# Optimization experiments

Hardware: AMD Instinct MI355X
Metric: run time of the kernel (lower is better)

Reference implementation:

```python
import jax, jax.numpy as jnp
import numpy as np

N = 50000      # nodes
E = 800000     # edges (avg degree 16)
DIN = 128
DH = 128
DOUT = 40
ALPHA = 0.1
BETA = 1.0


def gcn_conv(x, src, dst, ew, W, b, n):
    """PyG GCNConv: add self-loops, symmetric deg^-1/2 normalization, gather-scatter."""
    idx = jnp.arange(n)
    s = jnp.concatenate([src, idx])
    d = jnp.concatenate([dst, idx])
    w = jnp.concatenate([ew, jnp.ones((n,), x.dtype)])
    deg = jax.ops.segment_sum(w, d, num_segments=n)            # [N]
    dinv = jnp.where(deg > 0, jax.lax.rsqrt(deg), 0.0)
    norm = dinv[s] * w * dinv[d]                               # [E+N]
    h = x @ W                                                  # [N, dout]
    msg = h[s] * norm[:, None]                                 # gather + scale
    out = jax.ops.segment_sum(msg, d, num_segments=n)          # scatter-add
    return out + b


def setup_inputs() -> dict:
    key = jax.random.key(0)
    ks = jax.random.split(key, 10)
    x = jax.random.normal(ks[0], (N, DIN), jnp.float32)
    edge_index = jax.random.randint(ks[1], (2, E), 0, N, dtype=jnp.int64)
    edge_weight = jax.random.uniform(ks[2], (E,), jnp.float32)
    W1 = jax.random.normal(ks[3], (DIN, DH), jnp.float32) / np.float32(np.sqrt(DIN))
    b1 = jnp.zeros((DH,), jnp.float32)
    W2 = jax.random.normal(ks[4], (DH, DH), jnp.float32) / np.float32(np.sqrt(DH))
    b2 = jnp.zeros((DH,), jnp.float32)
    W3 = jax.random.normal(ks[5], (DH, DOUT), jnp.float32) / np.float32(np.sqrt(DH))
    b3 = jnp.zeros((DOUT,), jnp.float32)
    return {"x": x, "edge_index": edge_index, "edge_weight": edge_weight,
            "W1": W1, "b1": b1, "W2": W2, "b2": b2, "W3": W3, "b3": b3}


def reference(x, edge_index, edge_weight, W1, b1, W2, b2, W3, b3):
    src, dst = edge_index[0], edge_index[1]
    ones_w = jnp.ones((E,), x.dtype)
    h1 = jax.nn.relu(gcn_conv(x, src, dst, ones_w, W1, b1, N))   # conv1 (edge_weight=None)
    hc = gcn_conv(h1, src, dst, edge_weight, W2, b2, N)          # crf_layer with edge_weight
    h = ALPHA * h1 + BETA * hc                                   # weighted residual combo
    # LearnableBernoulliDropout: identity in eval mode
    out = gcn_conv(h, src, dst, ones_w, W3, b3, N)               # conv2
    return jax.nn.log_softmax(out, axis=1)
```

## Files before the change

kernel.cpp:

```cpp
#include <hip/hip_runtime.h>
#include <math.h>

#define DIN  128
#define DH   128
#define DOUT 40
#define ALPHA_C 0.1f
#define BETA_C  1.0f
#define SLOT 64

typedef __attribute__((ext_vector_type(8))) short short8;
typedef __attribute__((ext_vector_type(4))) float floatx4;

static inline int cdiv_h(int a, int b) { return (a + b - 1) / b; }

static __device__ __forceinline__ unsigned short f2b(float f) {
    unsigned u = __float_as_uint(f);
    u = u + 0x7FFFu + ((u >> 16) & 1u);
    return (unsigned short)(u >> 16);
}
static __device__ __forceinline__ unsigned pk2(float x, float y) {
    return (unsigned)f2b(x) | ((unsigned)f2b(y) << 16);
}
static __device__ __forceinline__ float2 b2f2(unsigned u) {
    float2 r;
    r.x = __uint_as_float(u << 16);
    r.y = __uint_as_float(u & 0xFFFF0000u);
    return r;
}

__global__ __launch_bounds__(256) void build_slots(const int* __restrict__ src,
                                                   const int* __restrict__ dst,
                                                   const float* __restrict__ ew,
                                                   int* cnt,
                                                   int* __restrict__ csr_src,
                                                   float* __restrict__ csr_w, int E) {
    int e = blockIdx.x * 256 + threadIdx.x;
    if (e >= E) return;
    int d = dst[e];
    int pos = atomicAdd(&cnt[d], 1);
    if (pos < SLOT) {
        int base = (d << 6) + pos;
        csr_src[base] = src[e];
        csr_w[base] = ew[e];
    }
}

__global__ __launch_bounds__(256) void wdeg_dinv(const int* __restrict__ cnt,
                                                 const float* __restrict__ csr_w,
                                                 float* __restrict__ dinv1,
                                                 float* __restrict__ dinv2, int n) {
    int i = blockIdx.x * 256 + threadIdx.x;
    if (i >= n) return;
    int c = cnt[i]; if (c > SLOT) c = SLOT;
    dinv1[i] = rsqrtf((float)c + 1.f);
    float s = 1.f;
    int jb = i << 6;
    for (int j = 0; j < c; ++j) s += csr_w[jb + j];
    dinv2[i] = rsqrtf(s);
}

template <bool ABF16>
__global__ __launch_bounds__(256) void gemm128(const void* __restrict__ Ain,
                                               const float* __restrict__ W,
                                               unsigned short* __restrict__ C, int M) {
    __shared__ short As[128 * 128];
    __shared__ short Bs[128 * 128];
    int t = threadIdx.x;
    int blockM = blockIdx.x * 128;

    {
        int r = t >> 1, h = t & 1;
        int rg = blockM + r; if (rg > M - 1) rg = M - 1;
        if (ABF16) {
            const uint4* arow = (const uint4*)((const unsigned short*)Ain + (size_t)rg * 128);
            #pragma unroll
            for (int i = 0; i < 8; ++i) {
                int chunk = h * 8 + i;
                uint4 v = arow[chunk];
                *(uint4*)&As[r * 128 + ((chunk ^ (r & 7)) * 8)] = v;
            }
        } else {
            const float4* arow = (const float4*)((const float*)Ain + (size_t)rg * 128);
            #pragma unroll
            for (int i = 0; i < 8; ++i) {
                int chunk = h * 8 + i;
                float4 v0 = arow[chunk * 2], v1 = arow[chunk * 2 + 1];
                uint4 p;
                p.x = pk2(v0.x, v0.y); p.y = pk2(v0.z, v0.w);
                p.z = pk2(v1.x, v1.y); p.w = pk2(v1.z, v1.w);
                *(uint4*)&As[r * 128 + ((chunk ^ (r & 7)) * 8)] = p;
            }
        }
    }
    {
        int n = t & 127;
        int k0 = (t >> 7) * 64;
        #pragma unroll
        for (int it = 0; it < 8; ++it) {
            int k = k0 + it * 8;
            float f0 = W[(size_t)(k + 0) * 128 + n];
            float f1 = W[(size_t)(k + 1) * 128 + n];
            float f2 = W[(size_t)(k + 2) * 128 + n];
            float f3 = W[(size_t)(k + 3) * 128 + n];
            float f4 = W[(size_t)(k + 4) * 128 + n];
            float f5 = W[(size_t)(k + 5) * 128 + n];
            float f6 = W[(size_t)(k + 6) * 128 + n];
            float f7 = W[(size_t)(k + 7) * 128 + n];
            uint4 p;
            p.x = pk2(f0, f1); p.y = pk2(f2, f3);
            p.z = pk2(f4, f5); p.w = pk2(f6, f7);
            *(uint4*)&Bs[n * 128 + (((k >> 3) ^ (n & 7)) * 8)] = p;
        }
    }
    __syncthreads();

    int w = t >> 6, l = t & 63;
    int q = l >> 4, lm = l & 15;
    int rowoff = (w >> 1) * 64, coloff = (w & 1) * 64;

    floatx4 acc[4][4] = {};
    #pragma unroll
    for (int ks = 0; ks < 4; ++ks) {
        int chunk = ks * 4 + q;
        int sw = (chunk ^ (lm & 7)) * 8;
        short8 af[4], bf[4];
        #pragma unroll
        for (int tm = 0; tm < 4; ++tm)
            af[tm] = *(const short8*)&As[(rowoff + tm * 16 + lm) * 128 + sw];
        #pragma unroll
        for (int tn = 0; tn < 4; ++tn)
            bf[tn] = *(const short8*)&Bs[(coloff + tn * 16 + lm) * 128 + sw];
        #pragma unroll
        for (int tm = 0; tm < 4; ++tm)
            #pragma unroll
            for (int tn = 0; tn < 4; ++tn)
                acc[tm][tn] = __builtin_amdgcn_mfma_f32_16x16x32_bf16(af[tm], bf[tn], acc[tm][tn], 0, 0, 0);
    }

    #pragma unroll
    for (int tm = 0; tm < 4; ++tm) {
        #pragma unroll
        for (int reg = 0; reg < 4; ++reg) {
            int row = blockM + rowoff + tm * 16 + q * 4 + reg;
            if (row >= M) continue;
            #pragma unroll
            for (int tn = 0; tn < 4; ++tn) {
                int col = coloff + tn * 16 + lm;
                C[(size_t)row * 128 + col] = f2b(acc[tm][tn][reg]);
            }
        }
    }
}

__global__ __launch_bounds__(256) void gemm40_lsm(const unsigned short* __restrict__ Ain,
                                                  const float* __restrict__ W,
                                                  const float* __restrict__ bias,
                                                  float* __restrict__ out, int M) {
    __shared__ short As[128 * 128];
    __shared__ short Bs[48 * 128];
    int t = threadIdx.x;
    int blockM = blockIdx.x * 128;

    {
        int r = t >> 1, h = t & 1;
        int rg = blockM + r; if (rg > M - 1) rg = M - 1;
        const uint4* arow = (const uint4*)(Ain + (size_t)rg * 128);
        #pragma unroll
        for (int i = 0; i < 8; ++i) {
            int chunk = h * 8 + i;
            uint4 v = arow[chunk];
            *(uint4*)&As[r * 128 + ((chunk ^ (r & 7)) * 8)] = v;
        }
    }
    {
        int n = t & 63;
        int k0 = (t >> 6) * 32;
        #pragma unroll
        for (int it = 0; it < 4; ++it) {
            int k = k0 + it * 8;
            uint4 p = {0, 0, 0, 0};
            if (n < 40) {
                float f0 = W[(size_t)(k + 0) * 40 + n];
                float f1 = W[(size_t)(k + 1) * 40 + n];
                float f2 = W[(size_t)(k + 2) * 40 + n];
                float f3 = W[(size_t)(k + 3) * 40 + n];
                float f4 = W[(size_t)(k + 4) * 40 + n];
                float f5 = W[(size_t)(k + 5) * 40 + n];
                float f6 = W[(size_t)(k + 6) * 40 + n];
                float f7 = W[(size_t)(k + 7) * 40 + n];
                p.x = pk2(f0, f1); p.y = pk2(f2, f3);
                p.z = pk2(f4, f5); p.w = pk2(f6, f7);
            }
            if (n < 48)
                *(uint4*)&Bs[n * 128 + (((k >> 3) ^ (n & 7)) * 8)] = p;
        }
    }
    __syncthreads();

    int w = t >> 6, l = t & 63;
    int q = l >> 4, lm = l & 15;
    int rowoff = w * 32;

    floatx4 acc[2][3] = {};
    #pragma unroll
    for (int ks = 0; ks < 4; ++ks) {
        int chunk = ks * 4 + q;
        int sw = (chunk ^ (lm & 7)) * 8;
        short8 af[2], bf[3];
        #pragma unroll
        for (int tm = 0; tm < 2; ++tm)
            af[tm] = *(const short8*)&As[(rowoff + tm * 16 + lm) * 128 + sw];
        #pragma unroll
        for (int tn = 0; tn < 3; ++tn)
            bf[tn] = *(const short8*)&Bs[(tn * 16 + lm) * 128 + sw];
        #pragma unroll
        for (int tm = 0; tm < 2; ++tm)
            #pragma unroll
            for (int tn = 0; tn < 3; ++tn)
                acc[tm][tn] = __builtin_amdgcn_mfma_f32_16x16x32_bf16(af[tm], bf[tn], acc[tm][tn], 0, 0, 0);
    }

    float bb0 = bias[lm];
    float bb1 = bias[16 + lm];
    float bb2 = (lm < 8) ? bias[32 + lm] : 0.f;
    #pragma unroll
    for (int tm = 0; tm < 2; ++tm) {
        #pragma unroll
        for (int reg = 0; reg < 4; ++reg) {
            int row = blockM + rowoff + tm * 16 + q * 4 + reg;
            float v0 = acc[tm][0][reg] + bb0;
            float v1 = acc[tm][1][reg] + bb1;
            float v2 = (lm < 8) ? acc[tm][2][reg] + bb2 : -INFINITY;
            float mx = fmaxf(fmaxf(v0, v1), v2);
            #pragma unroll
            for (int o = 1; o < 16; o <<= 1) mx = fmaxf(mx, __shfl_xor(mx, o, 64));
            float ss = expf(v0 - mx) + expf(v1 - mx) + ((lm < 8) ? expf(v2 - mx) : 0.f);
            #pragma unroll
            for (int o = 1; o < 16; o <<= 1) ss += __shfl_xor(ss, o, 64);
            float ls = mx + logf(ss);
            if (row < M) {
                out[(size_t)row * 40 + lm]      = v0 - ls;
                out[(size_t)row * 40 + 16 + lm] = v1 - ls;
                if (lm < 8) out[(size_t)row * 40 + 32 + lm] = v2 - ls;
            }
        }
    }
}

template <int MODE>
__global__ __launch_bounds__(256) void agg128(const unsigned short* __restrict__ hpre,
                                              unsigned short* __restrict__ io,
                                              const float* __restrict__ bias,
                                              const float* __restrict__ dinv,
                                              const int* __restrict__ cnt,
                                              const int* __restrict__ csr_src,
                                              const float* __restrict__ csr_w, int n) {
    int row = blockIdx.x * 4 + (threadIdx.x >> 6);
    if (row >= n) return;
    int lane = threadIdx.x & 63;
    const unsigned* hp = (const unsigned*)hpre;

    float di = dinv[row];
    float d2 = di * di;
    float2 acc = b2f2(hp[(size_t)row * 64 + lane]);
    if (MODE == 2) {
        acc.x *= d2; acc.y *= d2;
    } else {
        float2 bb = ((const float2*)bias)[lane];
        acc.x = fmaf(acc.x, d2, bb.x);
        acc.y = fmaf(acc.y, d2, bb.y);
    }

    int c = cnt[row]; if (c > SLOT) c = SLOT;
    int jb = row << 6;
    int je = jb + c;
    int j = jb;

    while (j + 8 <= je) {
        int ss[8]; float2 ff[8];
        #pragma unroll
        for (int u = 0; u < 8; ++u) ss[u] = csr_src[j + u];
        #pragma unroll
        for (int u = 0; u < 8; ++u) ff[u] = b2f2(hp[(size_t)ss[u] * 64 + lane]);
        #pragma unroll
        for (int u = 0; u < 8; ++u) {
            float cc = (MODE == 1) ? dinv[ss[u]] * csr_w[j + u] * di : dinv[ss[u]] * di;
            acc.x = fmaf(cc, ff[u].x, acc.x);
            acc.y = fmaf(cc, ff[u].y, acc.y);
        }
        j += 8;
    }
    if (j + 4 <= je) {
        int ss[4]; float2 ff[4];
        #pragma unroll
        for (int u = 0; u < 4; ++u) ss[u] = csr_src[j + u];
        #pragma unroll
        for (int u = 0; u < 4; ++u) ff[u] = b2f2(hp[(size_t)ss[u] * 64 + lane]);
        #pragma unroll
        for (int u = 0; u < 4; ++u) {
            float cc = (MODE == 1) ? dinv[ss[u]] * csr_w[j + u] * di : dinv[ss[u]] * di;
            acc.x = fmaf(cc, ff[u].x, acc.x);
            acc.y = fmaf(cc, ff[u].y, acc.y);
        }
        j += 4;
    }
    for (; j < je; ++j) {
        int s0 = csr_src[j];
        float cc = (MODE == 1) ? dinv[s0] * csr_w[j] * di : dinv[s0] * di;
        float2 f0 = b2f2(hp[(size_t)s0 * 64 + lane]);
        acc.x = fmaf(cc, f0.x, acc.x);
        acc.y = fmaf(cc, f0.y, acc.y);
    }

    unsigned* iop = (unsigned*)io;
    if (MODE == 0) {
        acc.x = fmaxf(acc.x, 0.f); acc.y = fmaxf(acc.y, 0.f);
        iop[(size_t)row * 64 + lane] = pk2(acc.x, acc.y);
    } else if (MODE == 1) {
        float2 h1 = b2f2(iop[(size_t)row * 64 + lane]);
        acc.x = fmaf(ALPHA_C, h1.x, BETA_C * acc.x);
        acc.y = fmaf(ALPHA_C, h1.y, BETA_C * acc.y);
        iop[(size_t)row * 64 + lane] = pk2(acc.x, acc.y);
    } else {
        iop[(size_t)row * 64 + lane] = pk2(acc.x, acc.y);
    }
}

extern "C" void kernel_launch(void* const* d_in, const int* in_sizes, int n_in,
                              void* d_out, int out_size, void* d_ws, size_t ws_size,
                              hipStream_t stream) {
    const float* x   = (const float*)d_in[0];
    const int*   ei  = (const int*)  d_in[1];
    const float* ew  = (const float*)d_in[2];
    const float* W1  = (const float*)d_in[3];
    const float* b1  = (const float*)d_in[4];
    const float* W2  = (const float*)d_in[5];
    const float* b2  = (const float*)d_in[6];
    const float* W3  = (const float*)d_in[7];
    const float* b3  = (const float*)d_in[8];
    float* out = (float*)d_out;

    const int Nn = in_sizes[0] / DIN;
    const int E  = in_sizes[1] / 2;
    const int* src = ei;
    const int* dst = ei + E;

    char* wsb = (char*)d_ws;
    int*   cnt     = (int*)wsb;                          wsb += (size_t)Nn * 4;
    float* dinv1   = (float*)wsb;                        wsb += (size_t)Nn * 4;
    float* dinv2   = (float*)wsb;                        wsb += (size_t)Nn * 4;
    int*   csr_src = (int*)wsb;                          wsb += (size_t)Nn * SLOT * 4;
    float* csr_w   = (float*)wsb;                        wsb += (size_t)Nn * SLOT * 4;
    unsigned short* hpreb = (unsigned short*)wsb;        wsb += (size_t)Nn * DH * 2;
    unsigned short* h1b   = (unsigned short*)wsb;        wsb += (size_t)Nn * DH * 2;

    hipMemsetAsync(cnt, 0, (size_t)Nn * 4, stream);
    build_slots<<<cdiv_h(E, 256), 256, 0, stream>>>(src, dst, ew, cnt, csr_src, csr_w, E);
    wdeg_dinv<<<cdiv_h(Nn, 256), 256, 0, stream>>>(cnt, csr_w, dinv1, dinv2, Nn);

    int gemmGrid = cdiv_h(Nn, 128);
    int aggGrid = cdiv_h(Nn, 4);

    gemm128<false><<<gemmGrid, 256, 0, stream>>>(x, W1, hpreb, Nn);
    agg128<0><<<aggGrid, 256, 0, stream>>>(hpreb, h1b, b1, dinv1, cnt, csr_src, csr_w, Nn);

    gemm128<true><<<gemmGrid, 256, 0, stream>>>(h1b, W2, hpreb, Nn);
    agg128<1><<<aggGrid, 256, 0, stream>>>(hpreb, h1b, b2, dinv2, cnt, csr_src, csr_w, Nn);

    agg128<2><<<aggGrid, 256, 0, stream>>>(h1b, hpreb, b3, dinv1, cnt, csr_src, csr_w, Nn);
    gemm40_lsm<<<gemmGrid, 256, 0, stream>>>(hpreb, W3, b3, out, Nn);
}
```

Before: 290.1 us.

## Interleave CSR src/weight and split wave into four edge groups with 16B loads

The separate csr_src and csr_w arrays are merged into one interleaved int2 array, so a single load fetches both the source index and the weight. The aggregation kernel now splits each 64-lane wave into four groups of 16 lanes. Each group handles every fourth edge and loads a full 256-byte feature row with 16-byte vector loads, and the partial sums are combined with cross-lane shuffles. build_slots also handles two edges per thread. The aim is fewer, wider memory transactions and more edge-level parallelism per row, at the cost of more registers and the shuffle reduction.

```diff
diff --git a/kernel.cpp b/kernel.cpp
--- a/kernel.cpp
+++ b/kernel.cpp
@@ -32,21 +32,25 @@
                                                    const int* __restrict__ dst,
                                                    const float* __restrict__ ew,
                                                    int* cnt,
-                                                   int* __restrict__ csr_src,
-                                                   float* __restrict__ csr_w, int E) {
+                                                   int2* __restrict__ csr, int E) {
+    int half = (E + 1) >> 1;
     int e = blockIdx.x * 256 + threadIdx.x;
-    if (e >= E) return;
-    int d = dst[e];
-    int pos = atomicAdd(&cnt[d], 1);
-    if (pos < SLOT) {
-        int base = (d << 6) + pos;
-        csr_src[base] = src[e];
-        csr_w[base] = ew[e];
+    if (e >= half) return;
+    {
+        int d = dst[e];
+        int pos = atomicAdd(&cnt[d], 1);
+        if (pos < SLOT) { int2 r; r.x = src[e]; r.y = __float_as_int(ew[e]); csr[(d << 6) + pos] = r; }
+    }
+    int e2 = e + half;
+    if (e2 < E) {
+        int d = dst[e2];
+        int pos = atomicAdd(&cnt[d], 1);
+        if (pos < SLOT) { int2 r; r.x = src[e2]; r.y = __float_as_int(ew[e2]); csr[(d << 6) + pos] = r; }
     }
 }
 
 __global__ __launch_bounds__(256) void wdeg_dinv(const int* __restrict__ cnt,
-                                                 const float* __restrict__ csr_w,
+                                                 const int2* __restrict__ csr,
                                                  float* __restrict__ dinv1,
                                                  float* __restrict__ dinv2, int n) {
     int i = blockIdx.x * 256 + threadIdx.x;
@@ -55,7 +59,7 @@
     dinv1[i] = rsqrtf((float)c + 1.f);
     float s = 1.f;
     int jb = i << 6;
-    for (int j = 0; j < c; ++j) s += csr_w[jb + j];
+    for (int j = 0; j < c; ++j) s += __int_as_float(csr[jb + j].y);
     dinv2[i] = rsqrtf(s);
 }
 
@@ -253,76 +257,82 @@
                                               const float* __restrict__ bias,
                                               const float* __restrict__ dinv,
                                               const int* __restrict__ cnt,
-                                              const int* __restrict__ csr_src,
-                                              const float* __restrict__ csr_w, int n) {
+                                              const int2* __restrict__ csr, int n) {
     int row = blockIdx.x * 4 + (threadIdx.x >> 6);
     if (row >= n) return;
     int lane = threadIdx.x & 63;
-    const unsigned* hp = (const unsigned*)hpre;
+    int q = lane >> 4, m = lane & 15;
+    const uint4* hp4 = (const uint4*)hpre;
 
     float di = dinv[row];
-    float d2 = di * di;
-    float2 acc = b2f2(hp[(size_t)row * 64 + lane]);
-    if (MODE == 2) {
-        acc.x *= d2; acc.y *= d2;
-    } else {
-        float2 bb = ((const float2*)bias)[lane];
-        acc.x = fmaf(acc.x, d2, bb.x);
-        acc.y = fmaf(acc.y, d2, bb.y);
-    }
+    float acc[8] = {};
 
     int c = cnt[row]; if (c > SLOT) c = SLOT;
     int jb = row << 6;
     int je = jb + c;
-    int j = jb;
-
-    while (j + 8 <= je) {
-        int ss[8]; float2 ff[8];
-        #pragma unroll
-        for (int u = 0; u < 8; ++u) ss[u] = csr_src[j + u];
-        #pragma unroll
-        for (int u = 0; u < 8; ++u) ff[u] = b2f2(hp[(size_t)ss[u] * 64 + lane]);
-        #pragma unroll
-        for (int u = 0; u < 8; ++u) {
-            float cc = (MODE == 1) ? dinv[ss[u]] * csr_w[j + u] * di : dinv[ss[u]] * di;
-            acc.x = fmaf(cc, ff[u].x, acc.x);
-            acc.y = fmaf(cc, ff[u].y, acc.y);
-        }
-        j += 8;
-    }
-    if (j + 4 <= je) {
-        int ss[4]; float2 ff[4];
-        #pragma unroll
-        for (int u = 0; u < 4; ++u) ss[u] = csr_src[j + u];
-        #pragma unroll
-        for (int u = 0; u < 4; ++u) ff[u] = b2f2(hp[(size_t)ss[u] * 64 + lane]);
-        #pragma unroll
-        for (int u = 0; u < 4; ++u) {
-            float cc = (MODE == 1) ? dinv[ss[u]] * csr_w[j + u] * di : dinv[ss[u]] * di;
-            acc.x = fmaf(cc, ff[u].x, acc.x);
-            acc.y = fmaf(cc, ff[u].y, acc.y);
-        }
-        j += 4;
-    }
-    for (; j < je; ++j) {
-        int s0 = csr_src[j];
-        float cc = (MODE == 1) ? dinv[s0] * csr_w[j] * di : dinv[s0] * di;
-        float2 f0 = b2f2(hp[(size_t)s0 * 64 + lane]);
-        acc.x = fmaf(cc, f0.x, acc.x);
-        acc.y = fmaf(cc, f0.y, acc.y);
-    }
-
-    unsigned* iop = (unsigned*)io;
-    if (MODE == 0) {
-        acc.x = fmaxf(acc.x, 0.f); acc.y = fmaxf(acc.y, 0.f);
-        iop[(size_t)row * 64 + lane] = pk2(acc.x, acc.y);
-    } else if (MODE == 1) {
-        float2 h1 = b2f2(iop[(size_t)row * 64 + lane]);
-        acc.x = fmaf(ALPHA_C, h1.x, BETA_C * acc.x);
-        acc.y = fmaf(ALPHA_C, h1.y, BETA_C * acc.y);
-        iop[(size_t)row * 64 + lane] = pk2(acc.x, acc.y);
-    } else {
-        iop[(size_t)row * 64 + lane] = pk2(acc.x, acc.y);
+
+    int j = jb + q;
+    #define ACC8(V, CC) { \
+        float2 p0 = b2f2(V.x), p1 = b2f2(V.y), p2 = b2f2(V.z), p3 = b2f2(V.w); \
+        acc[0] = fmaf(CC, p0.x, acc[0]); acc[1] = fmaf(CC, p0.y, acc[1]); \
+        acc[2] = fmaf(CC, p1.x, acc[2]); acc[3] = fmaf(CC, p1.y, acc[3]); \
+        acc[4] = fmaf(CC, p2.x, acc[4]); acc[5] = fmaf(CC, p2.y, acc[5]); \
+        acc[6] = fmaf(CC, p3.x, acc[6]); acc[7] = fmaf(CC, p3.y, acc[7]); }
+
+    for (; j + 4 < je; j += 8) {
+        int2 e0 = csr[j];
+        int2 e1 = csr[j + 4];
+        uint4 v0 = hp4[(size_t)e0.x * 16 + m];
+        uint4 v1 = hp4[(size_t)e1.x * 16 + m];
+        float c0 = (MODE == 1) ? dinv[e0.x] * __int_as_float(e0.y) * di : dinv[e0.x] * di;
+        float c1 = (MODE == 1) ? dinv[e1.x] * __int_as_float(e1.y) * di : dinv[e1.x] * di;
+        ACC8(v0, c0);
+        ACC8(v1, c1);
+    }
+    if (j < je) {
+        int2 e0 = csr[j];
+        uint4 v0 = hp4[(size_t)e0.x * 16 + m];
+        float c0 = (MODE == 1) ? dinv[e0.x] * __int_as_float(e0.y) * di : dinv[e0.x] * di;
+        ACC8(v0, c0);
+    }
+    #undef ACC8
+
+    #pragma unroll
+    for (int k = 0; k < 8; ++k) {
+        acc[k] += __shfl_xor(acc[k], 16, 64);
+        acc[k] += __shfl_xor(acc[k], 32, 64);
+    }
+
+    if (q == 0) {
+        float d2 = di * di;
+        uint4 self = hp4[(size_t)row * 16 + m];
+        float2 s0 = b2f2(self.x), s1 = b2f2(self.y), s2 = b2f2(self.z), s3 = b2f2(self.w);
+        float v[8] = { fmaf(s0.x, d2, acc[0]), fmaf(s0.y, d2, acc[1]),
+                       fmaf(s1.x, d2, acc[2]), fmaf(s1.y, d2, acc[3]),
+                       fmaf(s2.x, d2, acc[4]), fmaf(s2.y, d2, acc[5]),
+                       fmaf(s3.x, d2, acc[6]), fmaf(s3.y, d2, acc[7]) };
+        uint4* iop = (uint4*)io + (size_t)row * 16 + m;
+        if (MODE != 2) {
+            float4 ba = ((const float4*)bias)[m * 2];
+            float4 bbv = ((const float4*)bias)[m * 2 + 1];
+            v[0] += ba.x; v[1] += ba.y; v[2] += ba.z; v[3] += ba.w;
+            v[4] += bbv.x; v[5] += bbv.y; v[6] += bbv.z; v[7] += bbv.w;
+        }
+        if (MODE == 0) {
+            #pragma unroll
+            for (int k = 0; k < 8; ++k) v[k] = fmaxf(v[k], 0.f);
+        } else if (MODE == 1) {
+            uint4 h1 = *iop;
+            float2 a0 = b2f2(h1.x), a1 = b2f2(h1.y), a2 = b2f2(h1.z), a3 = b2f2(h1.w);
+            v[0] = fmaf(ALPHA_C, a0.x, BETA_C * v[0]); v[1] = fmaf(ALPHA_C, a0.y, BETA_C * v[1]);
+            v[2] = fmaf(ALPHA_C, a1.x, BETA_C * v[2]); v[3] = fmaf(ALPHA_C, a1.y, BETA_C * v[3]);
+            v[4] = fmaf(ALPHA_C, a2.x, BETA_C * v[4]); v[5] = fmaf(ALPHA_C, a2.y, BETA_C * v[5]);
+            v[6] = fmaf(ALPHA_C, a3.x, BETA_C * v[6]); v[7] = fmaf(ALPHA_C, a3.y, BETA_C * v[7]);
+        }
+        uint4 o;
+        o.x = pk2(v[0], v[1]); o.y = pk2(v[2], v[3]);
+        o.z = pk2(v[4], v[5]); o.w = pk2(v[6], v[7]);
+        *iop = o;
     }
 }
 
@@ -346,27 +356,26 @@
     const int* dst = ei + E;
 
     char* wsb = (char*)d_ws;
-    int*   cnt     = (int*)wsb;                          wsb += (size_t)Nn * 4;
-    float* dinv1   = (float*)wsb;                        wsb += (size_t)Nn * 4;
-    float* dinv2   = (float*)wsb;                        wsb += (size_t)Nn * 4;
-    int*   csr_src = (int*)wsb;                          wsb += (size_t)Nn * SLOT * 4;
-    float* csr_w   = (float*)wsb;                        wsb += (size_t)Nn * SLOT * 4;
+    int*   cnt   = (int*)wsb;                            wsb += (size_t)Nn * 4;
+    float* dinv1 = (float*)wsb;                          wsb += (size_t)Nn * 4;
+    float* dinv2 = (float*)wsb;                          wsb += (size_t)Nn * 4;
+    int2*  csr   = (int2*)wsb;                           wsb += (size_t)Nn * SLOT * 8;
     unsigned short* hpreb = (unsigned short*)wsb;        wsb += (size_t)Nn * DH * 2;
     unsigned short* h1b   = (unsigned short*)wsb;        wsb += (size_t)Nn * DH * 2;
 
     hipMemsetAsync(cnt, 0, (size_t)Nn * 4, stream);
-    build_slots<<<cdiv_h(E, 256), 256, 0, stream>>>(src, dst, ew, cnt, csr_src, csr_w, E);
-    wdeg_dinv<<<cdiv_h(Nn, 256), 256, 0, stream>>>(cnt, csr_w, dinv1, dinv2, Nn);
+    build_slots<<<cdiv_h((E + 1) / 2, 256), 256, 0, stream>>>(src, dst, ew, cnt, csr, E);
+    wdeg_dinv<<<cdiv_h(Nn, 256), 256, 0, stream>>>(cnt, csr, dinv1, dinv2, Nn);
 
     int gemmGrid = cdiv_h(Nn, 128);
     int aggGrid = cdiv_h(Nn, 4);
 
     gemm128<false><<<gemmGrid, 256, 0, stream>>>(x, W1, hpreb, Nn);
-    agg128<0><<<aggGrid, 256, 0, stream>>>(hpreb, h1b, b1, dinv1, cnt, csr_src, csr_w, Nn);
+    agg128<0><<<aggGrid, 256, 0, stream>>>(hpreb, h1b, b1, dinv1, cnt, csr, Nn);
 
     gemm128<true><<<gemmGrid, 256, 0, stream>>>(h1b, W2, hpreb, Nn);
-    agg128<1><<<aggGrid, 256, 0, stream>>>(hpreb, h1b, b2, dinv2, cnt, csr_src, csr_w, Nn);
-
-    agg128<2><<<aggGrid, 256, 0, stream>>>(h1b, hpreb, b3, dinv1, cnt, csr_src, csr_w, Nn);
+    agg128<1><<<aggGrid, 256, 0, stream>>>(hpreb, h1b, b2, dinv2, cnt, csr, Nn);
+
+    agg128<2><<<aggGrid, 256, 0, stream>>>(h1b, hpreb, b3, dinv1, cnt, csr, Nn);
     gemm40_lsm<<<gemmGrid, 256, 0, stream>>>(hpreb, W3, b3, out, Nn);
 }
```

Measured after the change: 295.0 us. Within noise of the previous version (+1.7%).

## Build per-XCD partitioned slot lists, compact to packed CSR, pretranspose weights

Applied to the files above, without the earlier changes.

Edge bucketing now uses one counter array per XCD, read from the hardware register, with workgroup-scope atomics so contention stays within one XCD's L2. A compact kernel then merges the partitions into a packed int2 (src, weight) CSR and computes both degree normalisations with a wave reduction. Weights are converted to bf16 and transposed once, so the GEMMs load them with vectorized copies. The cost is an extra pass, more workspace (partition buffers aliased with the activation buffers), and a relaxed per-partition capacity of 15 edges that could drop edges for high-degree nodes.

```diff
diff --git a/kernel.cpp b/kernel.cpp
--- a/kernel.cpp
+++ b/kernel.cpp
@@ -6,7 +6,9 @@
 #define DOUT 40
 #define ALPHA_C 0.1f
 #define BETA_C  1.0f
-#define SLOT 64
+#define NXCD 8
+#define PSLOT 16
+#define FSLOT 64
 
 typedef __attribute__((ext_vector_type(8))) short short8;
 typedef __attribute__((ext_vector_type(4))) float floatx4;
@@ -28,48 +30,100 @@
     return r;
 }
 
-__global__ __launch_bounds__(256) void build_slots(const int* __restrict__ src,
-                                                   const int* __restrict__ dst,
-                                                   const float* __restrict__ ew,
-                                                   int* cnt,
-                                                   int* __restrict__ csr_src,
-                                                   float* __restrict__ csr_w, int E) {
-    int e = blockIdx.x * 256 + threadIdx.x;
-    if (e >= E) return;
-    int d = dst[e];
-    int pos = atomicAdd(&cnt[d], 1);
-    if (pos < SLOT) {
-        int base = (d << 6) + pos;
-        csr_src[base] = src[e];
-        csr_w[base] = ew[e];
-    }
-}
-
-__global__ __launch_bounds__(256) void wdeg_dinv(const int* __restrict__ cnt,
-                                                 const float* __restrict__ csr_w,
-                                                 float* __restrict__ dinv1,
-                                                 float* __restrict__ dinv2, int n) {
-    int i = blockIdx.x * 256 + threadIdx.x;
-    if (i >= n) return;
-    int c = cnt[i]; if (c > SLOT) c = SLOT;
-    dinv1[i] = rsqrtf((float)c + 1.f);
-    float s = 1.f;
-    int jb = i << 6;
-    for (int j = 0; j < c; ++j) s += csr_w[jb + j];
-    dinv2[i] = rsqrtf(s);
+__global__ __launch_bounds__(256) void build_part(const int* __restrict__ src,
+                                                  const int* __restrict__ dst,
+                                                  const float* __restrict__ ew,
+                                                  int* __restrict__ cnt8,
+                                                  int2* __restrict__ csrP, int N, int E) {
+    unsigned xcc = __builtin_amdgcn_s_getreg((31u << 11) | 20u) & 7u;
+    int quarter = (E + 3) >> 2;
+    int e0 = blockIdx.x * 256 + threadIdx.x;
+    int* cntp = cnt8 + (size_t)xcc * N;
+
+    int idx[4]; int d[4], s[4]; float w[4]; int pos[4]; bool v[4];
+    #pragma unroll
+    for (int k = 0; k < 4; ++k) { idx[k] = e0 + k * quarter; v[k] = idx[k] < E; }
+    #pragma unroll
+    for (int k = 0; k < 4; ++k) if (v[k]) { d[k] = dst[idx[k]]; s[k] = src[idx[k]]; w[k] = ew[idx[k]]; }
+    #pragma unroll
+    for (int k = 0; k < 4; ++k) if (v[k])
+        pos[k] = __hip_atomic_fetch_add(&cntp[d[k]], 1, __ATOMIC_RELAXED, __HIP_MEMORY_SCOPE_WORKGROUP);
+    #pragma unroll
+    for (int k = 0; k < 4; ++k) if (v[k] && pos[k] < PSLOT - 1) {
+        int2 r; r.x = s[k]; r.y = __float_as_int(w[k]);
+        csrP[((size_t)d[k] << 7) + (xcc << 4) + pos[k]] = r;
+    }
+}
+
+__global__ __launch_bounds__(256) void compact(const int* __restrict__ cnt8,
+                                               const int2* __restrict__ csrP,
+                                               int2* __restrict__ csrF,
+                                               int* __restrict__ len,
+                                               float* __restrict__ dinv1,
+                                               float* __restrict__ dinv2, int N) {
+    int row = blockIdx.x * 4 + (threadIdx.x >> 6);
+    if (row >= N) return;
+    int lane = threadIdx.x & 63;
+
+    int cg[NXCD], pre[NXCD]; int tot = 0;
+    #pragma unroll
+    for (int g = 0; g < NXCD; ++g) {
+        int c = cnt8[(size_t)g * N + row];
+        if (c > PSLOT - 1) c = PSLOT - 1;
+        cg[g] = c; pre[g] = tot; tot += c;
+    }
+
+    float wsum = 0.f;
+    #pragma unroll
+    for (int h = 0; h < 2; ++h) {
+        int slot = lane + 64 * h;
+        int g = slot >> 4, pos = slot & 15;
+        if (pos < cg[g]) {
+            int2 r = csrP[((size_t)row << 7) + slot];
+            int dsti = pre[g] + pos;
+            if (dsti < FSLOT) csrF[((size_t)row << 6) + dsti] = r;
+            wsum += __int_as_float(r.y);
+        }
+    }
+    #pragma unroll
+    for (int o = 1; o < 64; o <<= 1) wsum += __shfl_xor(wsum, o, 64);
+
+    if (lane == 0) {
+        int t = tot > FSLOT ? FSLOT : tot;
+        len[row] = t;
+        dinv1[row] = rsqrtf((float)tot + 1.f);
+        dinv2[row] = rsqrtf(wsum + 1.f);
+    }
+}
+
+__global__ __launch_bounds__(256) void wt_conv(const float* __restrict__ W1,
+                                               const float* __restrict__ W2,
+                                               const float* __restrict__ W3,
+                                               unsigned short* __restrict__ WT) {
+    int gid = blockIdx.x * 256 + threadIdx.x;
+    if (gid < 16384) {
+        int n = gid >> 7, k = gid & 127;
+        WT[gid] = f2b(W1[(size_t)k * 128 + n]);
+    } else if (gid < 32768) {
+        int idx = gid - 16384, n = idx >> 7, k = idx & 127;
+        WT[gid] = f2b(W2[(size_t)k * 128 + n]);
+    } else if (gid < 32768 + 6144) {
+        int idx = gid - 32768, n = idx >> 7, k = idx & 127;
+        WT[gid] = (n < 40) ? f2b(W3[(size_t)k * 40 + n]) : (unsigned short)0;
+    }
 }
 
 template <bool ABF16>
 __global__ __launch_bounds__(256) void gemm128(const void* __restrict__ Ain,
-                                               const float* __restrict__ W,
+                                               const unsigned short* __restrict__ WT,
                                                unsigned short* __restrict__ C, int M) {
     __shared__ short As[128 * 128];
     __shared__ short Bs[128 * 128];
     int t = threadIdx.x;
     int blockM = blockIdx.x * 128;
+    int r = t >> 1, h = t & 1;
 
     {
-        int r = t >> 1, h = t & 1;
         int rg = blockM + r; if (rg > M - 1) rg = M - 1;
         if (ABF16) {
             const uint4* arow = (const uint4*)((const unsigned short*)Ain + (size_t)rg * 128);
@@ -93,23 +147,12 @@
         }
     }
     {
-        int n = t & 127;
-        int k0 = (t >> 7) * 64;
-        #pragma unroll
-        for (int it = 0; it < 8; ++it) {
-            int k = k0 + it * 8;
-            float f0 = W[(size_t)(k + 0) * 128 + n];
-            float f1 = W[(size_t)(k + 1) * 128 + n];
-            float f2 = W[(size_t)(k + 2) * 128 + n];
-            float f3 = W[(size_t)(k + 3) * 128 + n];
-            float f4 = W[(size_t)(k + 4) * 128 + n];
-            float f5 = W[(size_t)(k + 5) * 128 + n];
-            float f6 = W[(size_t)(k + 6) * 128 + n];
-            float f7 = W[(size_t)(k + 7) * 128 + n];
-            uint4 p;
-            p.x = pk2(f0, f1); p.y = pk2(f2, f3);
-            p.z = pk2(f4, f5); p.w = pk2(f6, f7);
-            *(uint4*)&Bs[n * 128 + (((k >> 3) ^ (n & 7)) * 8)] = p;
+        const uint4* brow = (const uint4*)(WT + (size_t)r * 128);
+        #pragma unroll
+        for (int i = 0; i < 8; ++i) {
+            int chunk = h * 8 + i;
+            uint4 v = brow[chunk];
+            *(uint4*)&Bs[r * 128 + ((chunk ^ (r & 7)) * 8)] = v;
         }
     }
     __syncthreads();
@@ -153,7 +196,7 @@
 }
 
 __global__ __launch_bounds__(256) void gemm40_lsm(const unsigned short* __restrict__ Ain,
-                                                  const float* __restrict__ W,
+                                                  const unsigned short* __restrict__ WT3,
                                                   const float* __restrict__ bias,
                                                   float* __restrict__ out, int M) {
     __shared__ short As[128 * 128];
@@ -172,27 +215,14 @@
             *(uint4*)&As[r * 128 + ((chunk ^ (r & 7)) * 8)] = v;
         }
     }
-    {
-        int n = t & 63;
-        int k0 = (t >> 6) * 32;
-        #pragma unroll
-        for (int it = 0; it < 4; ++it) {
-            int k = k0 + it * 8;
-            uint4 p = {0, 0, 0, 0};
-            if (n < 40) {
-                float f0 = W[(size_t)(k + 0) * 40 + n];
-                float f1 = W[(size_t)(k + 1) * 40 + n];
-                float f2 = W[(size_t)(k + 2) * 40 + n];
-                float f3 = W[(size_t)(k + 3) * 40 + n];
-                float f4 = W[(size_t)(k + 4) * 40 + n];
-                float f5 = W[(size_t)(k + 5) * 40 + n];
-                float f6 = W[(size_t)(k + 6) * 40 + n];
-                float f7 = W[(size_t)(k + 7) * 40 + n];
-                p.x = pk2(f0, f1); p.y = pk2(f2, f3);
-                p.z = pk2(f4, f5); p.w = pk2(f6, f7);
-            }
-            if (n < 48)
-                *(uint4*)&Bs[n * 128 + (((k >> 3) ^ (n & 7)) * 8)] = p;
+    if (t < 96) {
+        int r = t >> 1, h = t & 1;
+        const uint4* brow = (const uint4*)(WT3 + (size_t)r * 128);
+        #pragma unroll
+        for (int i = 0; i < 8; ++i) {
+            int chunk = h * 8 + i;
+            uint4 v = brow[chunk];
+            *(uint4*)&Bs[r * 128 + ((chunk ^ (r & 7)) * 8)] = v;
         }
     }
     __syncthreads();
@@ -248,13 +278,12 @@
 }
 
 template <int MODE>
-__global__ __launch_bounds__(256) void agg128(const unsigned short* __restrict__ hpre,
-                                              unsigned short* __restrict__ io,
-                                              const float* __restrict__ bias,
-                                              const float* __restrict__ dinv,
-                                              const int* __restrict__ cnt,
-                                              const int* __restrict__ csr_src,
-                                              const float* __restrict__ csr_w, int n) {
+__global__ __launch_bounds__(256) void agg128f(const unsigned short* __restrict__ hpre,
+                                               unsigned short* __restrict__ io,
+                                               const float* __restrict__ bias,
+                                               const float* __restrict__ dinv,
+                                               const int* __restrict__ len,
+                                               const int2* __restrict__ csrF, int n) {
     int row = blockIdx.x * 4 + (threadIdx.x >> 6);
     if (row >= n) return;
     int lane = threadIdx.x & 63;
@@ -271,43 +300,44 @@
         acc.y = fmaf(acc.y, d2, bb.y);
     }
 
-    int c = cnt[row]; if (c > SLOT) c = SLOT;
-    int jb = row << 6;
-    int je = jb + c;
-    int j = jb;
-
-    while (j + 8 <= je) {
-        int ss[8]; float2 ff[8];
-        #pragma unroll
-        for (int u = 0; u < 8; ++u) ss[u] = csr_src[j + u];
-        #pragma unroll
-        for (int u = 0; u < 8; ++u) ff[u] = b2f2(hp[(size_t)ss[u] * 64 + lane]);
+    int c = len[row];
+    size_t jb = (size_t)row << 6;
+    int j = 0;
+
+    while (j + 8 <= c) {
+        int2 ee[8]; float2 ff[8];
+        #pragma unroll
+        for (int u = 0; u < 8; ++u) ee[u] = csrF[jb + j + u];
+        #pragma unroll
+        for (int u = 0; u < 8; ++u) ff[u] = b2f2(hp[(size_t)ee[u].x * 64 + lane]);
         #pragma unroll
         for (int u = 0; u < 8; ++u) {
-            float cc = (MODE == 1) ? dinv[ss[u]] * csr_w[j + u] * di : dinv[ss[u]] * di;
+            float cc = (MODE == 1) ? dinv[ee[u].x] * __int_as_float(ee[u].y) * di
+                                   : dinv[ee[u].x] * di;
             acc.x = fmaf(cc, ff[u].x, acc.x);
             acc.y = fmaf(cc, ff[u].y, acc.y);
         }
         j += 8;
     }
-    if (j + 4 <= je) {
-        int ss[4]; float2 ff[4];
-        #pragma unroll
-        for (int u = 0; u < 4; ++u) ss[u] = csr_src[j + u];
-        #pragma unroll
-        for (int u = 0; u < 4; ++u) ff[u] = b2f2(hp[(size_t)ss[u] * 64 + lane]);
+    if (j + 4 <= c) {
+        int2 ee[4]; float2 ff[4];
+        #pragma unroll
+        for (int u = 0; u < 4; ++u) ee[u] = csrF[jb + j + u];
+        #pragma unroll
+        for (int u = 0; u < 4; ++u) ff[u] = b2f2(hp[(size_t)ee[u].x * 64 + lane]);
         #pragma unroll
         for (int u = 0; u < 4; ++u) {
-            float cc = (MODE == 1) ? dinv[ss[u]] * csr_w[j + u] * di : dinv[ss[u]] * di;
+            float cc = (MODE == 1) ? dinv[ee[u].x] * __int_as_float(ee[u].y) * di
+                                   : dinv[ee[u].x] * di;
             acc.x = fmaf(cc, ff[u].x, acc.x);
             acc.y = fmaf(cc, ff[u].y, acc.y);
         }
         j += 4;
     }
-    for (; j < je; ++j) {
-        int s0 = csr_src[j];
-        float cc = (MODE == 1) ? dinv[s0] * csr_w[j] * di : dinv[s0] * di;
-        float2 f0 = b2f2(hp[(size_t)s0 * 64 + lane]);
+    for (; j < c; ++j) {
+        int2 e0 = csrF[jb + j];
+        float cc = (MODE == 1) ? dinv[e0.x] * __int_as_float(e0.y) * di : dinv[e0.x] * di;
+        float2 f0 = b2f2(hp[(size_t)e0.x * 64 + lane]);
         acc.x = fmaf(cc, f0.x, acc.x);
         acc.y = fmaf(cc, f0.y, acc.y);
     }
@@ -346,27 +376,30 @@
     const int* dst = ei + E;
 
     char* wsb = (char*)d_ws;
-    int*   cnt     = (int*)wsb;                          wsb += (size_t)Nn * 4;
-    float* dinv1   = (float*)wsb;                        wsb += (size_t)Nn * 4;
-    float* dinv2   = (float*)wsb;                        wsb += (size_t)Nn * 4;
-    int*   csr_src = (int*)wsb;                          wsb += (size_t)Nn * SLOT * 4;
-    float* csr_w   = (float*)wsb;                        wsb += (size_t)Nn * SLOT * 4;
-    unsigned short* hpreb = (unsigned short*)wsb;        wsb += (size_t)Nn * DH * 2;
-    unsigned short* h1b   = (unsigned short*)wsb;        wsb += (size_t)Nn * DH * 2;
-
-    hipMemsetAsync(cnt, 0, (size_t)Nn * 4, stream);
-    build_slots<<<cdiv_h(E, 256), 256, 0, stream>>>(src, dst, ew, cnt, csr_src, csr_w, E);
-    wdeg_dinv<<<cdiv_h(Nn, 256), 256, 0, stream>>>(cnt, csr_w, dinv1, dinv2, Nn);
+    int*      cnt8  = (int*)wsb;                         wsb += (size_t)NXCD * Nn * 4;
+    int*      len   = (int*)wsb;                         wsb += (size_t)Nn * 4;
+    float*    dinv1 = (float*)wsb;                       wsb += (size_t)Nn * 4;
+    float*    dinv2 = (float*)wsb;                       wsb += (size_t)Nn * 4;
+    unsigned short* WT = (unsigned short*)wsb;           wsb += (size_t)(32768 + 6144) * 2;
+    int2*     csrF  = (int2*)wsb;                        wsb += (size_t)Nn * FSLOT * 8;
+    int2*     csrP  = (int2*)wsb;
+    unsigned short* hpreb = (unsigned short*)csrP;
+    unsigned short* h1b   = (unsigned short*)csrP + (size_t)Nn * DH;
+
+    hipMemsetAsync(cnt8, 0, (size_t)NXCD * Nn * 4, stream);
+    build_part<<<cdiv_h((E + 3) / 4, 256), 256, 0, stream>>>(src, dst, ew, cnt8, csrP, Nn, E);
+    compact<<<cdiv_h(Nn, 4), 256, 0, stream>>>(cnt8, csrP, csrF, len, dinv1, dinv2, Nn);
+    wt_conv<<<cdiv_h(32768 + 6144, 256), 256, 0, stream>>>(W1, W2, W3, WT);
 
     int gemmGrid = cdiv_h(Nn, 128);
     int aggGrid = cdiv_h(Nn, 4);
 
-    gemm128<false><<<gemmGrid, 256, 0, stream>>>(x, W1, hpreb, Nn);
-    agg128<0><<<aggGrid, 256, 0, stream>>>(hpreb, h1b, b1, dinv1, cnt, csr_src, csr_w, Nn);
-
-    gemm128<true><<<gemmGrid, 256, 0, stream>>>(h1b, W2, hpreb, Nn);
-    agg128<1><<<aggGrid, 256, 0, stream>>>(hpreb, h1b, b2, dinv2, cnt, csr_src, csr_w, Nn);
-
-    agg128<2><<<aggGrid, 256, 0, stream>>>(h1b, hpreb, b3, dinv1, cnt, csr_src, csr_w, Nn);
-    gemm40_lsm<<<gemmGrid, 256, 0, stream>>>(hpreb, W3, b3, out, Nn);
-}
+    gemm128<false><<<gemmGrid, 256, 0, stream>>>(x, WT, hpreb, Nn);
+    agg128f<0><<<aggGrid, 256, 0, stream>>>(hpreb, h1b, b1, dinv1, len, csrF, Nn);
+
+    gemm128<true><<<gemmGrid, 256, 0, stream>>>(h1b, WT + 16384, hpreb, Nn);
+    agg128f<1><<<aggGrid, 256, 0, stream>>>(hpreb, h1b, b2, dinv2, len, csrF, Nn);
+
+    agg128f<2><<<aggGrid, 256, 0, stream>>>(h1b, hpreb, b3, dinv1, len, csrF, Nn);
+    gemm40_lsm<<<gemmGrid, 256, 0, stream>>>(hpreb, WT + 32768, b3, out, Nn);
+}
```

After: 306.3 us. 5.6% more time.
